# Kernel optimization log

Measured on AMD Instinct MI355X. Metric: run time of the kernel, lower is better.

Reference implementation:

```python
import jax, jax.numpy as jnp
import numpy as np

DIM = 512
HEADS = 8
DIM_HEAD = 64
INNER = HEADS * DIM_HEAD  # 512


def setup_inputs() -> dict:
    key = jax.random.key(0)
    ks = jax.random.split(key, 6)
    B, N = 8, 1024
    x = jax.random.normal(ks[0], (B, N, DIM), dtype=jnp.float32)
    w_qkv = jax.random.normal(ks[1], (DIM, 3 * INNER), dtype=jnp.float32) * (DIM ** -0.5)
    reattn_weights = jax.random.normal(ks[2], (HEADS, HEADS), dtype=jnp.float32)
    ln_gamma = jnp.ones((HEADS,), dtype=jnp.float32)
    ln_beta = jnp.zeros((HEADS,), dtype=jnp.float32)
    w_out = jax.random.normal(ks[3], (INNER, DIM), dtype=jnp.float32) * (INNER ** -0.5)
    b_out = jnp.zeros((DIM,), dtype=jnp.float32)
    return {"x": x, "w_qkv": w_qkv, "reattn_weights": reattn_weights,
            "ln_gamma": ln_gamma, "ln_beta": ln_beta, "w_out": w_out, "b_out": b_out}


def reference(x, w_qkv, reattn_weights, ln_gamma, ln_beta, w_out, b_out):
    B, N, C = x.shape
    scale = DIM_HEAD ** -0.5
    qkv = (x @ w_qkv).reshape(B, N, 3, HEADS, DIM_HEAD)
    qkv = jnp.transpose(qkv, (2, 0, 3, 1, 4))  # [3, B, H, N, D]
    q, k, v = qkv[0], qkv[1], qkv[2]
    dots = jnp.einsum('bhid,bhjd->bhij', q, k) * scale
    attn = jax.nn.softmax(dots, axis=-1)
    # cross-head re-mixing
    attn = jnp.einsum('bhij,hg->bgij', attn, reattn_weights)
    # LayerNorm over the head axis per (b, i, j)
    mean = jnp.mean(attn, axis=1, keepdims=True)
    var = jnp.var(attn, axis=1, keepdims=True)
    attn = (attn - mean) * jax.lax.rsqrt(var + 1e-5)
    attn = attn * ln_gamma[None, :, None, None] + ln_beta[None, :, None, None]
    out = jnp.einsum('bhij,bhjd->bhid', attn, v)
    out = jnp.transpose(out, (0, 2, 1, 3)).reshape(B, N, INNER)
    return out @ w_out + b_out
```

## Files before the change

### kernel.cpp

```cpp
#include <hip/hip_runtime.h>
#include <hip/hip_bf16.h>
#include <stdint.h>


#define DIMC 512

typedef __attribute__((ext_vector_type(8))) short bf16x8;
typedef __attribute__((ext_vector_type(4))) float f32x4;
typedef __attribute__((ext_vector_type(8))) unsigned short u16x8;

__device__ __forceinline__ unsigned short f2bf(float f) {
    union { float f; uint32_t u; } v; v.f = f;
    uint32_t u = v.u;
    return (unsigned short)((u + 0x7fffu + ((u >> 16) & 1u)) >> 16);
}
__device__ __forceinline__ float bf2f(unsigned short s) {
    union { uint32_t u; float f; } v; v.u = ((uint32_t)s) << 16;
    return v.f;
}

#define MFMA(a, b, c) __builtin_amdgcn_mfma_f32_16x16x32_bf16((a), (b), (c), 0, 0, 0)

#define GLOAD16(gptr, lptr)                                                        \
    __builtin_amdgcn_global_load_lds((const __attribute__((address_space(1))) void*)(gptr), \
                                     (__attribute__((address_space(3))) void*)(lptr), 16, 0, 0)

__global__ void k_conv(const float* __restrict__ in, unsigned short* __restrict__ out, int n8) {
    int t = blockIdx.x * blockDim.x + threadIdx.x;
    if (t >= n8) return;
    const float4* p = reinterpret_cast<const float4*>(in) + (size_t)t * 2;
    float4 a = p[0], b = p[1];
    u16x8 o;
    o[0] = f2bf(a.x); o[1] = f2bf(a.y); o[2] = f2bf(a.z); o[3] = f2bf(a.w);
    o[4] = f2bf(b.x); o[5] = f2bf(b.y); o[6] = f2bf(b.z); o[7] = f2bf(b.w);
    *(reinterpret_cast<u16x8*>(out) + t) = o;
}

__global__ __launch_bounds__(256) void k_tconv(const float* __restrict__ in,
                                               unsigned short* __restrict__ out, int R, int C) {
    __shared__ float tile[64][65];
    int ct = C >> 6;
    int bx = blockIdx.x % ct;
    int by = blockIdx.x / ct;
    int r0 = by * 64, c0 = bx * 64;
    int tx = threadIdx.x & 63, ty = threadIdx.x >> 6;
#pragma unroll
    for (int rr = 0; rr < 16; rr++) {
        int row = ty + rr * 4;
        tile[row][tx] = in[(size_t)(r0 + row) * C + c0 + tx];
    }
    __syncthreads();
#pragma unroll
    for (int rr = 0; rr < 16; rr++) {
        int row = ty + rr * 4;
        out[(size_t)(c0 + row) * R + r0 + tx] = f2bf(tile[tx][row]);
    }
}

__global__ __launch_bounds__(256) void k_qkv(const unsigned short* __restrict__ A,
                                             const unsigned short* __restrict__ BT,
                                             unsigned short* __restrict__ q,
                                             unsigned short* __restrict__ kk,
                                             unsigned short* __restrict__ vv) {
    __shared__ unsigned short Al[128 * 32];
    __shared__ unsigned short Bl[128 * 32];
    int mt = blockIdx.x / 12, nt = blockIdx.x % 12;
    int m0 = mt * 128, c0 = nt * 128;
    int tid = threadIdx.x, lane = tid & 63, w = tid >> 6;
    int wr = w >> 1, wc = w & 1;
    int lr = lane & 15, lb = lane >> 4;
    f32x4 acc[4][4] = {};
    const unsigned short* gA = A + (size_t)(m0 + 32 * w + (lane >> 2)) * DIMC + (lane & 3) * 8;
    const unsigned short* gB = BT + (size_t)(c0 + 32 * w + (lane >> 2)) * DIMC + (lane & 3) * 8;
    char* lA = (char*)Al + w * 2048;
    char* lB = (char*)Bl + w * 2048;
    for (int k0 = 0; k0 < DIMC; k0 += 32) {
        __syncthreads();
        GLOAD16(gA + k0, lA);
        GLOAD16(gA + k0 + 16 * DIMC, lA + 1024);
        GLOAD16(gB + k0, lB);
        GLOAD16(gB + k0 + 16 * DIMC, lB + 1024);
        __syncthreads();
        bf16x8 af[4], bfr[4];
#pragma unroll
        for (int mi = 0; mi < 4; mi++)
            af[mi] = *reinterpret_cast<const bf16x8*>(&Al[(64 * wr + 16 * mi + lr) * 32 + 8 * lb]);
#pragma unroll
        for (int ni = 0; ni < 4; ni++)
            bfr[ni] = *reinterpret_cast<const bf16x8*>(&Bl[(64 * wc + 16 * ni + lr) * 32 + 8 * lb]);
#pragma unroll
        for (int mi = 0; mi < 4; mi++)
#pragma unroll
            for (int ni = 0; ni < 4; ni++)
                acc[mi][ni] = MFMA(af[mi], bfr[ni], acc[mi][ni]);
    }
#pragma unroll
    for (int ni = 0; ni < 4; ni++) {
        int c = c0 + 64 * wc + 16 * ni + lr;
        int which = c >> 9, rem = c & 511, h = rem >> 6, d = rem & 63;
        unsigned short* dst = which == 0 ? q : (which == 1 ? kk : vv);
        float sc = which == 0 ? 0.125f : 1.0f;
#pragma unroll
        for (int mi = 0; mi < 4; mi++) {
#pragma unroll
            for (int r = 0; r < 4; r++) {
                int m = m0 + 64 * wr + 16 * mi + 4 * lb + r;
                int b = m >> 10, n = m & 1023;
                dst[(((size_t)(b * 8 + h) * 1024) + n) * 64 + d] = f2bf(acc[mi][ni][r] * sc);
            }
        }
    }
}

__global__ __launch_bounds__(256) void k_vtrans(const unsigned short* __restrict__ v,
                                                unsigned short* __restrict__ vT) {
    __shared__ unsigned short tile[64][72];
    int bh = blockIdx.x >> 4;
    int n0 = (blockIdx.x & 15) * 64;
    int t = threadIdx.x;
    int nl = t >> 2, c4 = t & 3;
    const u16x8* src = reinterpret_cast<const u16x8*>(v + ((size_t)bh * 1024 + n0 + nl) * 64 + c4 * 16);
    u16x8 x0 = src[0], x1 = src[1];
    *reinterpret_cast<u16x8*>(&tile[nl][c4 * 16]) = x0;
    *reinterpret_cast<u16x8*>(&tile[nl][c4 * 16 + 8]) = x1;
    __syncthreads();
    int dl = t >> 2, n4 = t & 3;
#pragma unroll
    for (int c = 0; c < 2; c++) {
        u16x8 o;
#pragma unroll
        for (int i = 0; i < 8; i++) o[i] = tile[n4 * 16 + 8 * c + i][dl];
        *reinterpret_cast<u16x8*>(vT + ((size_t)bh * 64 + dl) * 1024 + n0 + n4 * 16 + 8 * c) = o;
    }
}

__global__ __launch_bounds__(256) void k_ml(const unsigned short* __restrict__ q,
                                            const unsigned short* __restrict__ kk,
                                            float* __restrict__ m_out,
                                            float* __restrict__ linv_out) {
    int it = blockIdx.x & 63;
    int bh = blockIdx.x >> 6;
    int i0 = it * 16;
    int lane = threadIdx.x & 63, w = threadIdx.x >> 6;
    int lr = lane & 15, lb = lane >> 4;
    const unsigned short* qp = q + (size_t)bh * 1024 * 64;
    const unsigned short* kp = kk + (size_t)bh * 1024 * 64;
    f32x4 acc[16] = {};
    bf16x8 a0 = *reinterpret_cast<const bf16x8*>(qp + (size_t)(i0 + lr) * 64 + 0 + 8 * lb);
    bf16x8 a1 = *reinterpret_cast<const bf16x8*>(qp + (size_t)(i0 + lr) * 64 + 32 + 8 * lb);
#pragma unroll
    for (int t = 0; t < 16; t++) {
        int j0 = w * 256 + t * 16;
        bf16x8 b0 = *reinterpret_cast<const bf16x8*>(kp + (size_t)(j0 + lr) * 64 + 0 + 8 * lb);
        acc[t] = MFMA(a0, b0, acc[t]);
        bf16x8 b1 = *reinterpret_cast<const bf16x8*>(kp + (size_t)(j0 + lr) * 64 + 32 + 8 * lb);
        acc[t] = MFMA(a1, b1, acc[t]);
    }
    __shared__ float red[4][16];
    float mx[4], sm[4];
#pragma unroll
    for (int r = 0; r < 4; r++) {
        float m = acc[0][r];
#pragma unroll
        for (int t = 1; t < 16; t++) m = fmaxf(m, acc[t][r]);
        for (int off = 1; off < 16; off <<= 1) m = fmaxf(m, __shfl_xor(m, off));
        mx[r] = m;
    }
    if (lr == 0) {
#pragma unroll
        for (int r = 0; r < 4; r++) red[w][4 * lb + r] = mx[r];
    }
    __syncthreads();
#pragma unroll
    for (int r = 0; r < 4; r++) {
        int row = 4 * lb + r;
        mx[r] = fmaxf(fmaxf(red[0][row], red[1][row]), fmaxf(red[2][row], red[3][row]));
    }
    __syncthreads();
#pragma unroll
    for (int r = 0; r < 4; r++) {
        float s = 0.f;
#pragma unroll
        for (int t = 0; t < 16; t++) s += __expf(acc[t][r] - mx[r]);
        for (int off = 1; off < 16; off <<= 1) s += __shfl_xor(s, off);
        sm[r] = s;
    }
    if (lr == 0) {
#pragma unroll
        for (int r = 0; r < 4; r++) red[w][4 * lb + r] = sm[r];
    }
    __syncthreads();
    if (w == 0 && lr == 0) {
#pragma unroll
        for (int r = 0; r < 4; r++) {
            int row = 4 * lb + r;
            float tot = red[0][row] + red[1][row] + red[2][row] + red[3][row];
            m_out[(size_t)bh * 1024 + i0 + row] = mx[r];
            linv_out[(size_t)bh * 1024 + i0 + row] = 1.0f / tot;
        }
    }
}

__global__ __launch_bounds__(512) void k_fused(const unsigned short* __restrict__ q,
                                               const unsigned short* __restrict__ kk,
                                               const unsigned short* __restrict__ vT,
                                               const float* __restrict__ m_arr,
                                               const float* __restrict__ l_arr,
                                               const float* __restrict__ W,
                                               const float* __restrict__ gamma,
                                               const float* __restrict__ beta,
                                               unsigned short* __restrict__ outh) {
    __shared__ float P[8][16 * 65];
    __shared__ unsigned short PM[8][16 * 72];
    int b = blockIdx.x >> 6, it = blockIdx.x & 63, i0 = it * 16;
    int tid = threadIdx.x, h = tid >> 6, lane = tid & 63;
    int lr = lane & 15, lb = lane >> 4;
    int bh = b * 8 + h;
    const unsigned short* qp = q + (size_t)bh * 65536;
    const unsigned short* kp = kk + (size_t)bh * 65536;
    const unsigned short* vp = vT + (size_t)bh * 65536;
    bf16x8 aq0 = *reinterpret_cast<const bf16x8*>(qp + (size_t)(i0 + lr) * 64 + 8 * lb);
    bf16x8 aq1 = *reinterpret_cast<const bf16x8*>(qp + (size_t)(i0 + lr) * 64 + 32 + 8 * lb);
    float mr[4], li[4];
#pragma unroll
    for (int r = 0; r < 4; r++) {
        mr[r] = m_arr[(size_t)bh * 1024 + i0 + 4 * lb + r];
        li[r] = l_arr[(size_t)bh * 1024 + i0 + 4 * lb + r];
    }
    float wv[64];
#pragma unroll
    for (int x = 0; x < 64; x++) wv[x] = W[x];
    float gv[8], bv[8];
#pragma unroll
    for (int x = 0; x < 8; x++) { gv[x] = gamma[x]; bv[x] = beta[x]; }
    f32x4 accO[4] = {};
    int mj = tid & 63;
    int mi0 = tid >> 6;
    for (int jt = 0; jt < 16; jt++) {
        int j0 = jt * 64;
        f32x4 s[4] = {};
#pragma unroll
        for (int f = 0; f < 4; f++) {
            bf16x8 bk0 = *reinterpret_cast<const bf16x8*>(kp + (size_t)(j0 + 16 * f + lr) * 64 + 8 * lb);
            s[f] = MFMA(aq0, bk0, s[f]);
            bf16x8 bk1 = *reinterpret_cast<const bf16x8*>(kp + (size_t)(j0 + 16 * f + lr) * 64 + 32 + 8 * lb);
            s[f] = MFMA(aq1, bk1, s[f]);
        }
#pragma unroll
        for (int f = 0; f < 4; f++)
#pragma unroll
            for (int r = 0; r < 4; r++)
                P[h][(4 * lb + r) * 65 + 16 * f + lr] = __expf(s[f][r] - mr[r]) * li[r];
        __syncthreads();
#pragma unroll
        for (int e = 0; e < 2; e++) {
            int il = mi0 + 8 * e;
            float av[8];
#pragma unroll
            for (int hh = 0; hh < 8; hh++) av[hh] = P[hh][il * 65 + mj];
            float mg[8], sum = 0.f;
#pragma unroll
            for (int g = 0; g < 8; g++) {
                float m = 0.f;
#pragma unroll
                for (int hh = 0; hh < 8; hh++) m += av[hh] * wv[hh * 8 + g];
                mg[g] = m; sum += m;
            }
            float mean = sum * 0.125f;
            float ss = 0.f;
#pragma unroll
            for (int g = 0; g < 8; g++) { float d = mg[g] - mean; ss += d * d; }
            float rs = rsqrtf(ss * 0.125f + 1e-5f);
#pragma unroll
            for (int g = 0; g < 8; g++)
                PM[g][il * 72 + mj] = f2bf((mg[g] - mean) * rs * gv[g] + bv[g]);
        }
        __syncthreads();
#pragma unroll
        for (int kc = 0; kc < 2; kc++) {
            bf16x8 ap = *reinterpret_cast<const bf16x8*>(&PM[h][lr * 72 + 32 * kc + 8 * lb]);
#pragma unroll
            for (int df = 0; df < 4; df++) {
                bf16x8 bvv = *reinterpret_cast<const bf16x8*>(vp + (size_t)(16 * df + lr) * 1024 + j0 + 32 * kc + 8 * lb);
                accO[df] = MFMA(ap, bvv, accO[df]);
            }
        }
    }
#pragma unroll
    for (int df = 0; df < 4; df++) {
#pragma unroll
        for (int r = 0; r < 4; r++) {
            int i = i0 + 4 * lb + r;
            outh[((size_t)(b * 1024 + i)) * 512 + h * 64 + 16 * df + lr] = f2bf(accO[df][r]);
        }
    }
}

__global__ __launch_bounds__(256) void k_proj(const unsigned short* __restrict__ A,
                                              const unsigned short* __restrict__ BT,
                                              const float* __restrict__ bias,
                                              float* __restrict__ out) {
    __shared__ unsigned short Al[128 * 32];
    __shared__ unsigned short Bl[128 * 32];
    int mt = blockIdx.x >> 2, nt = blockIdx.x & 3;
    int m0 = mt * 128, c0 = nt * 128;
    int tid = threadIdx.x, lane = tid & 63, w = tid >> 6;
    int wr = w >> 1, wc = w & 1;
    int lr = lane & 15, lb = lane >> 4;
    f32x4 acc[4][4] = {};
    const unsigned short* gA = A + (size_t)(m0 + 32 * w + (lane >> 2)) * DIMC + (lane & 3) * 8;
    const unsigned short* gB = BT + (size_t)(c0 + 32 * w + (lane >> 2)) * DIMC + (lane & 3) * 8;
    char* lA = (char*)Al + w * 2048;
    char* lB = (char*)Bl + w * 2048;
    for (int k0 = 0; k0 < DIMC; k0 += 32) {
        __syncthreads();
        GLOAD16(gA + k0, lA);
        GLOAD16(gA + k0 + 16 * DIMC, lA + 1024);
        GLOAD16(gB + k0, lB);
        GLOAD16(gB + k0 + 16 * DIMC, lB + 1024);
        __syncthreads();
        bf16x8 af[4], bfr[4];
#pragma unroll
        for (int mi = 0; mi < 4; mi++)
            af[mi] = *reinterpret_cast<const bf16x8*>(&Al[(64 * wr + 16 * mi + lr) * 32 + 8 * lb]);
#pragma unroll
        for (int ni = 0; ni < 4; ni++)
            bfr[ni] = *reinterpret_cast<const bf16x8*>(&Bl[(64 * wc + 16 * ni + lr) * 32 + 8 * lb]);
#pragma unroll
        for (int mi = 0; mi < 4; mi++)
#pragma unroll
            for (int ni = 0; ni < 4; ni++)
                acc[mi][ni] = MFMA(af[mi], bfr[ni], acc[mi][ni]);
    }
#pragma unroll
    for (int ni = 0; ni < 4; ni++) {
        int c = c0 + 64 * wc + 16 * ni + lr;
        float bs = bias[c];
#pragma unroll
        for (int mi = 0; mi < 4; mi++) {
#pragma unroll
            for (int r = 0; r < 4; r++) {
                int m = m0 + 64 * wr + 16 * mi + 4 * lb + r;
                out[(size_t)m * 512 + c] = acc[mi][ni][r] + bs;
            }
        }
    }
}

extern "C" void kernel_launch(void* const* d_in, const int* in_sizes, int n_in,
                              void* d_out, int out_size, void* d_ws, size_t ws_size,
                              hipStream_t stream) {
    (void)in_sizes; (void)n_in; (void)out_size; (void)ws_size;
    const float* x      = (const float*)d_in[0];
    const float* w_qkv  = (const float*)d_in[1];
    const float* W      = (const float*)d_in[2];
    const float* gamma  = (const float*)d_in[3];
    const float* beta   = (const float*)d_in[4];
    const float* w_out  = (const float*)d_in[5];
    const float* b_out  = (const float*)d_in[6];
    float* out = (float*)d_out;

    char* ws = (char*)d_ws;
    unsigned short* xb   = (unsigned short*)(ws + 0);
    unsigned short* wbT  = (unsigned short*)(ws + 8388608);
    unsigned short* w_oT = (unsigned short*)(ws + 9961472);
    unsigned short* q    = (unsigned short*)(ws + 10485760);
    unsigned short* k    = (unsigned short*)(ws + 18874368);
    unsigned short* v    = (unsigned short*)(ws + 27262976);
    unsigned short* vT   = (unsigned short*)(ws + 35651584);
    unsigned short* outh = (unsigned short*)(ws + 44040192);
    float* m_arr         = (float*)(ws + 52428800);
    float* l_arr         = (float*)(ws + 52690944);

    k_conv<<<2048, 256, 0, stream>>>(x, xb, 8192 * 512 / 8);
    k_tconv<<<(512 / 64) * (1536 / 64), 256, 0, stream>>>(w_qkv, wbT, 512, 1536);
    k_tconv<<<(512 / 64) * (512 / 64), 256, 0, stream>>>(w_out, w_oT, 512, 512);
    k_qkv<<<(8192 / 128) * (1536 / 128), 256, 0, stream>>>(xb, wbT, q, k, v);
    k_vtrans<<<64 * 16, 256, 0, stream>>>(v, vT);
    k_ml<<<64 * 64, 256, 0, stream>>>(q, k, m_arr, l_arr);
    k_fused<<<8 * 64, 512, 0, stream>>>(q, k, vT, m_arr, l_arr, W, gamma, beta, outh);
    k_proj<<<(8192 / 128) * (512 / 128), 256, 0, stream>>>(outh, w_oT, b_out, out);
}
```

Baseline: 324.7 us.

## Materialize normalized softmax probabilities in bf16 and pipeline head-mix with PV

Replaces the separate row-max/sum kernel and the fused kernel that recomputed QK^T with one kernel that computes QK^T once, does the full softmax and writes bf16 probabilities to a 128 MB workspace buffer. A second kernel streams those probabilities into LDS with async global-to-LDS loads, prefetching the next tile while the current one is used, then applies the head mixing and LayerNorm (mean taken through precomputed column sums of the mixing weights) into a swizzled LDS tile for the PV MFMAs. This removes the duplicated QK^T matmul and exponentials. In exchange it adds a large HBM write and read of the probability matrix and rounds the probabilities to bf16 before the mixing step.

```diff
diff --git a/kernel.cpp b/kernel.cpp
--- a/kernel.cpp
+++ b/kernel.cpp
@@ -13,10 +13,6 @@
     union { float f; uint32_t u; } v; v.f = f;
     uint32_t u = v.u;
     return (unsigned short)((u + 0x7fffu + ((u >> 16) & 1u)) >> 16);
-}
-__device__ __forceinline__ float bf2f(unsigned short s) {
-    union { uint32_t u; float f; } v; v.u = ((uint32_t)s) << 16;
-    return v.f;
 }
 
 #define MFMA(a, b, c) __builtin_amdgcn_mfma_f32_16x16x32_bf16((a), (b), (c), 0, 0, 0)
@@ -134,166 +130,219 @@
     }
 }
 
-__global__ __launch_bounds__(256) void k_ml(const unsigned short* __restrict__ q,
-                                            const unsigned short* __restrict__ kk,
-                                            float* __restrict__ m_out,
-                                            float* __restrict__ linv_out) {
-    int it = blockIdx.x & 63;
-    int bh = blockIdx.x >> 6;
-    int i0 = it * 16;
-    int lane = threadIdx.x & 63, w = threadIdx.x >> 6;
+__global__ __launch_bounds__(512) void k_attn(const unsigned short* __restrict__ q,
+                                              const unsigned short* __restrict__ kk,
+                                              unsigned short* __restrict__ P) {
+    __shared__ float redm[32][8];
+    __shared__ float redl[32][8];
+    int blk = blockIdx.x;
+    int bh = blk & 63, it = blk >> 6;
+    int i0 = it * 32;
+    int tid = threadIdx.x, w = tid >> 6, lane = tid & 63;
     int lr = lane & 15, lb = lane >> 4;
-    const unsigned short* qp = q + (size_t)bh * 1024 * 64;
-    const unsigned short* kp = kk + (size_t)bh * 1024 * 64;
-    f32x4 acc[16] = {};
-    bf16x8 a0 = *reinterpret_cast<const bf16x8*>(qp + (size_t)(i0 + lr) * 64 + 0 + 8 * lb);
-    bf16x8 a1 = *reinterpret_cast<const bf16x8*>(qp + (size_t)(i0 + lr) * 64 + 32 + 8 * lb);
-#pragma unroll
-    for (int t = 0; t < 16; t++) {
-        int j0 = w * 256 + t * 16;
-        bf16x8 b0 = *reinterpret_cast<const bf16x8*>(kp + (size_t)(j0 + lr) * 64 + 0 + 8 * lb);
-        acc[t] = MFMA(a0, b0, acc[t]);
-        bf16x8 b1 = *reinterpret_cast<const bf16x8*>(kp + (size_t)(j0 + lr) * 64 + 32 + 8 * lb);
-        acc[t] = MFMA(a1, b1, acc[t]);
-    }
-    __shared__ float red[4][16];
-    float mx[4], sm[4];
-#pragma unroll
-    for (int r = 0; r < 4; r++) {
-        float m = acc[0][r];
-#pragma unroll
-        for (int t = 1; t < 16; t++) m = fmaxf(m, acc[t][r]);
-        for (int off = 1; off < 16; off <<= 1) m = fmaxf(m, __shfl_xor(m, off));
-        mx[r] = m;
-    }
+    int j0 = w * 128;
+    const unsigned short* qp = q + (size_t)bh * 65536;
+    const unsigned short* kp = kk + (size_t)bh * 65536;
+    bf16x8 aq[2][2];
+#pragma unroll
+    for (int mf = 0; mf < 2; mf++)
+#pragma unroll
+        for (int ks = 0; ks < 2; ks++)
+            aq[mf][ks] = *reinterpret_cast<const bf16x8*>(qp + (size_t)(i0 + 16 * mf + lr) * 64 + 32 * ks + 8 * lb);
+    f32x4 acc[2][8] = {};
+#pragma unroll
+    for (int nf = 0; nf < 8; nf++) {
+#pragma unroll
+        for (int ks = 0; ks < 2; ks++) {
+            bf16x8 bk = *reinterpret_cast<const bf16x8*>(kp + (size_t)(j0 + 16 * nf + lr) * 64 + 32 * ks + 8 * lb);
+            acc[0][nf] = MFMA(aq[0][ks], bk, acc[0][nf]);
+            acc[1][nf] = MFMA(aq[1][ks], bk, acc[1][nf]);
+        }
+    }
+    float mfin[2][4];
+#pragma unroll
+    for (int mf = 0; mf < 2; mf++)
+#pragma unroll
+        for (int r = 0; r < 4; r++) {
+            float m = acc[mf][0][r];
+#pragma unroll
+            for (int nf = 1; nf < 8; nf++) m = fmaxf(m, acc[mf][nf][r]);
+            m = fmaxf(m, __shfl_xor(m, 1)); m = fmaxf(m, __shfl_xor(m, 2));
+            m = fmaxf(m, __shfl_xor(m, 4)); m = fmaxf(m, __shfl_xor(m, 8));
+            mfin[mf][r] = m;
+        }
     if (lr == 0) {
 #pragma unroll
-        for (int r = 0; r < 4; r++) red[w][4 * lb + r] = mx[r];
-    }
-    __syncthreads();
-#pragma unroll
-    for (int r = 0; r < 4; r++) {
-        int row = 4 * lb + r;
-        mx[r] = fmaxf(fmaxf(red[0][row], red[1][row]), fmaxf(red[2][row], red[3][row]));
-    }
-    __syncthreads();
-#pragma unroll
-    for (int r = 0; r < 4; r++) {
-        float s = 0.f;
-#pragma unroll
-        for (int t = 0; t < 16; t++) s += __expf(acc[t][r] - mx[r]);
-        for (int off = 1; off < 16; off <<= 1) s += __shfl_xor(s, off);
-        sm[r] = s;
-    }
+        for (int mf = 0; mf < 2; mf++)
+#pragma unroll
+            for (int r = 0; r < 4; r++) redm[16 * mf + 4 * lb + r][w] = mfin[mf][r];
+    }
+    __syncthreads();
+#pragma unroll
+    for (int mf = 0; mf < 2; mf++)
+#pragma unroll
+        for (int r = 0; r < 4; r++) {
+            int row = 16 * mf + 4 * lb + r;
+            float m = redm[row][0];
+#pragma unroll
+            for (int ww = 1; ww < 8; ww++) m = fmaxf(m, redm[row][ww]);
+            mfin[mf][r] = m;
+        }
+    float lfin[2][4];
+#pragma unroll
+    for (int mf = 0; mf < 2; mf++)
+#pragma unroll
+        for (int r = 0; r < 4; r++) {
+            float s = 0.f;
+#pragma unroll
+            for (int nf = 0; nf < 8; nf++) {
+                float e = __expf(acc[mf][nf][r] - mfin[mf][r]);
+                acc[mf][nf][r] = e;
+                s += e;
+            }
+            s += __shfl_xor(s, 1); s += __shfl_xor(s, 2);
+            s += __shfl_xor(s, 4); s += __shfl_xor(s, 8);
+            lfin[mf][r] = s;
+        }
     if (lr == 0) {
 #pragma unroll
-        for (int r = 0; r < 4; r++) red[w][4 * lb + r] = sm[r];
-    }
-    __syncthreads();
-    if (w == 0 && lr == 0) {
+        for (int mf = 0; mf < 2; mf++)
+#pragma unroll
+            for (int r = 0; r < 4; r++) redl[16 * mf + 4 * lb + r][w] = lfin[mf][r];
+    }
+    __syncthreads();
+#pragma unroll
+    for (int mf = 0; mf < 2; mf++)
 #pragma unroll
         for (int r = 0; r < 4; r++) {
-            int row = 4 * lb + r;
-            float tot = red[0][row] + red[1][row] + red[2][row] + red[3][row];
-            m_out[(size_t)bh * 1024 + i0 + row] = mx[r];
-            linv_out[(size_t)bh * 1024 + i0 + row] = 1.0f / tot;
-        }
-    }
-}
-
-__global__ __launch_bounds__(512) void k_fused(const unsigned short* __restrict__ q,
-                                               const unsigned short* __restrict__ kk,
+            int row = 16 * mf + 4 * lb + r;
+            float s = 0.f;
+#pragma unroll
+            for (int ww = 0; ww < 8; ww++) s += redl[row][ww];
+            lfin[mf][r] = 1.0f / s;
+        }
+    unsigned short* pp = P + (size_t)bh * 1048576;
+#pragma unroll
+    for (int mf = 0; mf < 2; mf++)
+#pragma unroll
+        for (int nf = 0; nf < 8; nf++)
+#pragma unroll
+            for (int r = 0; r < 4; r++)
+                pp[(size_t)(i0 + 16 * mf + 4 * lb + r) * 1024 + j0 + 16 * nf + lr] =
+                    f2bf(acc[mf][nf][r] * lfin[mf][r]);
+}
+
+__global__ __launch_bounds__(512) void k_mixpv(const unsigned short* __restrict__ P,
                                                const unsigned short* __restrict__ vT,
-                                               const float* __restrict__ m_arr,
-                                               const float* __restrict__ l_arr,
-                                               const float* __restrict__ W,
+                                               const float* __restrict__ Wm,
                                                const float* __restrict__ gamma,
                                                const float* __restrict__ beta,
                                                unsigned short* __restrict__ outh) {
-    __shared__ float P[8][16 * 65];
-    __shared__ unsigned short PM[8][16 * 72];
-    int b = blockIdx.x >> 6, it = blockIdx.x & 63, i0 = it * 16;
-    int tid = threadIdx.x, h = tid >> 6, lane = tid & 63;
+    __shared__ unsigned short Pex[8 * 1024];
+    __shared__ unsigned short PMl[8 * 1024];
+    int blk = blockIdx.x;
+    int b = blk & 7, it = blk >> 3;
+    int i0 = it * 16;
+    int tid = threadIdx.x, w = tid >> 6, lane = tid & 63;
     int lr = lane & 15, lb = lane >> 4;
-    int bh = b * 8 + h;
-    const unsigned short* qp = q + (size_t)bh * 65536;
-    const unsigned short* kp = kk + (size_t)bh * 65536;
-    const unsigned short* vp = vT + (size_t)bh * 65536;
-    bf16x8 aq0 = *reinterpret_cast<const bf16x8*>(qp + (size_t)(i0 + lr) * 64 + 8 * lb);
-    bf16x8 aq1 = *reinterpret_cast<const bf16x8*>(qp + (size_t)(i0 + lr) * 64 + 32 + 8 * lb);
-    float mr[4], li[4];
-#pragma unroll
-    for (int r = 0; r < 4; r++) {
-        mr[r] = m_arr[(size_t)bh * 1024 + i0 + 4 * lb + r];
-        li[r] = l_arr[(size_t)bh * 1024 + i0 + 4 * lb + r];
-    }
     float wv[64];
 #pragma unroll
-    for (int x = 0; x < 64; x++) wv[x] = W[x];
-    float gv[8], bv[8];
-#pragma unroll
-    for (int x = 0; x < 8; x++) { gv[x] = gamma[x]; bv[x] = beta[x]; }
+    for (int x2 = 0; x2 < 64; x2++) wv[x2] = Wm[x2];
+    float cv[8];
+#pragma unroll
+    for (int h = 0; h < 8; h++) {
+        float s = 0.f;
+#pragma unroll
+        for (int g = 0; g < 8; g++) s += wv[h * 8 + g];
+        cv[h] = s * 0.125f;
+    }
+    float gv[8], bvv[8];
+#pragma unroll
+    for (int x2 = 0; x2 < 8; x2++) { gv[x2] = gamma[x2]; bvv[x2] = beta[x2]; }
+    const unsigned short* pbase = P + (size_t)(b * 8 + w) * 1048576 + (size_t)i0 * 1024;
+    const unsigned short* vp = vT + (size_t)(b * 8 + w) * 65536;
+    int ii = tid >> 5;
+    int jj = (tid & 31) * 2;
     f32x4 accO[4] = {};
-    int mj = tid & 63;
-    int mi0 = tid >> 6;
+
+    auto PH1 = [&](int jt) {
+        int j0 = jt * 64;
+#pragma unroll
+        for (int c = 0; c < 2; c++) {
+            int o = c * 512 + lane * 8;
+            GLOAD16(pbase + (size_t)(o >> 6) * 1024 + j0 + (o & 63),
+                    (char*)Pex + w * 2048 + c * 1024);
+        }
+    };
+    auto PH2 = [&]() {
+        float alo[8], ahi[8];
+#pragma unroll
+        for (int h = 0; h < 8; h++) {
+            uint32_t pv = *reinterpret_cast<const uint32_t*>(Pex + h * 1024 + ii * 64 + jj);
+            alo[h] = __uint_as_float(pv << 16);
+            ahi[h] = __uint_as_float(pv & 0xffff0000u);
+        }
+        float mgl[8], mgh[8];
+        float meanl = 0.f, meanh = 0.f;
+#pragma unroll
+        for (int g = 0; g < 8; g++) {
+            float sl = 0.f, sh = 0.f;
+#pragma unroll
+            for (int h = 0; h < 8; h++) { sl += alo[h] * wv[h * 8 + g]; sh += ahi[h] * wv[h * 8 + g]; }
+            mgl[g] = sl; mgh[g] = sh;
+        }
+#pragma unroll
+        for (int h = 0; h < 8; h++) { meanl += alo[h] * cv[h]; meanh += ahi[h] * cv[h]; }
+        float vl = 0.f, vh = 0.f;
+#pragma unroll
+        for (int g = 0; g < 8; g++) {
+            float dl = mgl[g] - meanl, dh = mgh[g] - meanh;
+            vl += dl * dl; vh += dh * dh;
+        }
+        float rl = rsqrtf(vl * 0.125f + 1e-5f), rh = rsqrtf(vh * 0.125f + 1e-5f);
+#pragma unroll
+        for (int g = 0; g < 8; g++) {
+            unsigned short ol = f2bf((mgl[g] - meanl) * rl * gv[g] + bvv[g]);
+            unsigned short oh = f2bf((mgh[g] - meanh) * rh * gv[g] + bvv[g]);
+            uint32_t pk = (uint32_t)ol | ((uint32_t)oh << 16);
+            int byteoff = (g * 2048 + ii * 128 + jj * 2) ^ ((ii & 7) << 4);
+            *reinterpret_cast<uint32_t*>((char*)PMl + byteoff) = pk;
+        }
+    };
+    auto PH3 = [&](int jt) {
+        int j0 = jt * 64;
+        bf16x8 Af[2];
+#pragma unroll
+        for (int kc = 0; kc < 2; kc++) {
+            int byteoff = (w * 2048 + lr * 128 + kc * 64 + lb * 16) ^ ((lr & 7) << 4);
+            Af[kc] = *reinterpret_cast<const bf16x8*>((const char*)PMl + byteoff);
+        }
+#pragma unroll
+        for (int kc = 0; kc < 2; kc++)
+#pragma unroll
+            for (int df = 0; df < 4; df++) {
+                bf16x8 bv8 = *reinterpret_cast<const bf16x8*>(vp + (size_t)(16 * df + lr) * 1024 + j0 + 32 * kc + 8 * lb);
+                accO[df] = MFMA(Af[kc], bv8, accO[df]);
+            }
+    };
+
+    PH1(0);
+    __syncthreads();
+    PH2();
+    __syncthreads();
     for (int jt = 0; jt < 16; jt++) {
-        int j0 = jt * 64;
-        f32x4 s[4] = {};
-#pragma unroll
-        for (int f = 0; f < 4; f++) {
-            bf16x8 bk0 = *reinterpret_cast<const bf16x8*>(kp + (size_t)(j0 + 16 * f + lr) * 64 + 8 * lb);
-            s[f] = MFMA(aq0, bk0, s[f]);
-            bf16x8 bk1 = *reinterpret_cast<const bf16x8*>(kp + (size_t)(j0 + 16 * f + lr) * 64 + 32 + 8 * lb);
-            s[f] = MFMA(aq1, bk1, s[f]);
-        }
-#pragma unroll
-        for (int f = 0; f < 4; f++)
-#pragma unroll
-            for (int r = 0; r < 4; r++)
-                P[h][(4 * lb + r) * 65 + 16 * f + lr] = __expf(s[f][r] - mr[r]) * li[r];
-        __syncthreads();
-#pragma unroll
-        for (int e = 0; e < 2; e++) {
-            int il = mi0 + 8 * e;
-            float av[8];
-#pragma unroll
-            for (int hh = 0; hh < 8; hh++) av[hh] = P[hh][il * 65 + mj];
-            float mg[8], sum = 0.f;
-#pragma unroll
-            for (int g = 0; g < 8; g++) {
-                float m = 0.f;
-#pragma unroll
-                for (int hh = 0; hh < 8; hh++) m += av[hh] * wv[hh * 8 + g];
-                mg[g] = m; sum += m;
-            }
-            float mean = sum * 0.125f;
-            float ss = 0.f;
-#pragma unroll
-            for (int g = 0; g < 8; g++) { float d = mg[g] - mean; ss += d * d; }
-            float rs = rsqrtf(ss * 0.125f + 1e-5f);
-#pragma unroll
-            for (int g = 0; g < 8; g++)
-                PM[g][il * 72 + mj] = f2bf((mg[g] - mean) * rs * gv[g] + bv[g]);
-        }
-        __syncthreads();
-#pragma unroll
-        for (int kc = 0; kc < 2; kc++) {
-            bf16x8 ap = *reinterpret_cast<const bf16x8*>(&PM[h][lr * 72 + 32 * kc + 8 * lb]);
-#pragma unroll
-            for (int df = 0; df < 4; df++) {
-                bf16x8 bvv = *reinterpret_cast<const bf16x8*>(vp + (size_t)(16 * df + lr) * 1024 + j0 + 32 * kc + 8 * lb);
-                accO[df] = MFMA(ap, bvv, accO[df]);
-            }
-        }
-    }
-#pragma unroll
-    for (int df = 0; df < 4; df++) {
-#pragma unroll
-        for (int r = 0; r < 4; r++) {
-            int i = i0 + 4 * lb + r;
-            outh[((size_t)(b * 1024 + i)) * 512 + h * 64 + 16 * df + lr] = f2bf(accO[df][r]);
-        }
-    }
+        if (jt < 15) PH1(jt + 1);
+        PH3(jt);
+        __syncthreads();
+        if (jt < 15) PH2();
+        __syncthreads();
+    }
+    int bi = b * 1024 + i0;
+#pragma unroll
+    for (int df = 0; df < 4; df++)
+#pragma unroll
+        for (int r = 0; r < 4; r++)
+            outh[(size_t)(bi + 4 * lb + r) * 512 + w * 64 + 16 * df + lr] = f2bf(accO[df][r]);
 }
 
 __global__ __launch_bounds__(256) void k_proj(const unsigned short* __restrict__ A,
@@ -369,15 +418,14 @@
     unsigned short* v    = (unsigned short*)(ws + 27262976);
     unsigned short* vT   = (unsigned short*)(ws + 35651584);
     unsigned short* outh = (unsigned short*)(ws + 44040192);
-    float* m_arr         = (float*)(ws + 52428800);
-    float* l_arr         = (float*)(ws + 52690944);
+    unsigned short* P    = (unsigned short*)(ws + 52428800);
 
     k_conv<<<2048, 256, 0, stream>>>(x, xb, 8192 * 512 / 8);
     k_tconv<<<(512 / 64) * (1536 / 64), 256, 0, stream>>>(w_qkv, wbT, 512, 1536);
     k_tconv<<<(512 / 64) * (512 / 64), 256, 0, stream>>>(w_out, w_oT, 512, 512);
     k_qkv<<<(8192 / 128) * (1536 / 128), 256, 0, stream>>>(xb, wbT, q, k, v);
     k_vtrans<<<64 * 16, 256, 0, stream>>>(v, vT);
-    k_ml<<<64 * 64, 256, 0, stream>>>(q, k, m_arr, l_arr);
-    k_fused<<<8 * 64, 512, 0, stream>>>(q, k, vT, m_arr, l_arr, W, gamma, beta, outh);
+    k_attn<<<64 * 32, 512, 0, stream>>>(q, k, P);
+    k_mixpv<<<8 * 64, 512, 0, stream>>>(P, vT, W, gamma, beta, outh);
     k_proj<<<(8192 / 128) * (512 / 128), 256, 0, stream>>>(outh, w_oT, b_out, out);
 }
```

New measurement: 260.5 us. 19.8% less time.
